# Kernel tuning notes

Hardware: AMD Instinct MI355X
Metric: run time of the kernel (lower is better)

## Reference

```python
import jax, jax.numpy as jnp
import numpy as np

BUFFER_C = 1.25

def setup_inputs() -> dict:
    key = jax.random.key(0)
    k1, k2, k3 = jax.random.split(key, 3)
    T, D, E = 4096, 1024, 8
    x = jax.random.normal(k1, (T, D), dtype=jnp.float32)
    Wg = jax.random.normal(k2, (D, E), dtype=jnp.float32) / np.sqrt(D)
    bg = jnp.zeros((E,), dtype=jnp.float32)
    W = jax.random.normal(k3, (E, D, D), dtype=jnp.float32) / np.sqrt(D)
    b = jnp.zeros((E, D), dtype=jnp.float32)
    return {"x": x, "Wg": Wg, "bg": bg, "W": W, "b": b}


def reference(x, Wg, bg, W, b):
    # Top-1 (Switch-style) routing with capacity buffer, per-expert Linear,
    # prob-weighted combine, plus load-balancing aux loss.
    T, D = x.shape
    E = W.shape[0]
    capacity = int(BUFFER_C * T / E)

    logits = x @ Wg + bg                      # [T, E]
    probs = jax.nn.softmax(logits, axis=-1)   # [T, E]
    top_idx = jnp.argmax(probs, axis=-1)      # [T]
    top_prob = jnp.take_along_axis(probs, top_idx[:, None], axis=-1)[:, 0]

    onehot = jax.nn.one_hot(top_idx, E, dtype=x.dtype)       # [T, E]
    # 1-indexed position of each token within its expert's buffer
    pos = jnp.cumsum(onehot, axis=0) * onehot                # [T, E]
    dispatch = jnp.where((onehot > 0) & (pos <= capacity), 1.0, 0.0).astype(x.dtype)

    # dense dispatch/combine equivalent of the masked per-expert loop
    xe = jnp.einsum('te,td->etd', dispatch, x)               # [E, T, D]
    ye = jnp.einsum('etd,edf->etf', xe, W) + b[:, None, :]   # [E, T, D]
    y = jnp.einsum('te,etf->tf', dispatch, ye)               # [T, D] (0 for dropped)
    out = y * top_prob[:, None]

    # aux load-balance loss: E * sum_e f_e * P_e
    f = onehot.mean(axis=0)
    P = probs.mean(axis=0)
    aux_loss = E * jnp.sum(f * P)
    return out, aux_loss
```

## Files before the change

### kernel.cpp

```cpp
#include <hip/hip_runtime.h>
#include <hip/hip_bf16.h>
#include <cstdint>

#define T_TOK 4096
#define D_DIM 1024
#define E_EXP 8
#define CAP   640
#define MAXDROP 3456
#define MT    10
#define GBLK  1024
#define NSUB  32

typedef __attribute__((ext_vector_type(8))) short short8;
typedef __attribute__((ext_vector_type(4))) float f32x4;

__device__ inline unsigned short f2bf(float f) {
    uint32_t u = __float_as_uint(f);
    u += 0x7fffu + ((u >> 16) & 1u);
    return (unsigned short)(u >> 16);
}

__device__ inline void dma16(const void* g, void* l) {
    __builtin_amdgcn_global_load_lds(
        (const __attribute__((address_space(1))) unsigned int*)g,
        (__attribute__((address_space(3))) unsigned int*)l, 16, 0, 0);
}

#define WB_TILE(e, nt, kt) ((((size_t)(e) * 16 + (nt)) * 16 + (kt)) * 4096)
#define XG_TILE(e, mt, kt) ((((size_t)(e) * MT + (mt)) * 16 + (kt)) * 4096)

__global__ __launch_bounds__(256) void prep_kernel(
    const float* __restrict__ x, const float* __restrict__ Wg,
    const float* __restrict__ bg, const float* __restrict__ W,
    unsigned short* __restrict__ Wb,
    int* __restrict__ top_idx, float* __restrict__ top_prob,
    float* __restrict__ blkpart)
{
    int bid = blockIdx.x;
    int tid = threadIdx.x;

    if (bid >= GBLK) {
        int bid2 = (bid - GBLK) * 2;
        int e   = bid2 >> 8;
        int kt  = (bid2 >> 4) & 15;
        int ntA = bid2 & 15;
        int k0  = kt * 64;
        const float* Wsrc = W + (size_t)e * D_DIM * D_DIM + (size_t)k0 * D_DIM;

        int c0 = tid, c1 = tid + 256;
        int g0 = c0 >> 6, n0c = c0 & 63;
        int g1 = c1 >> 6, n1c = c1 & 63;

        #pragma unroll
        for (int half = 0; half < 2; half++) {
            int n0 = (ntA + half) * 64;
            unsigned short* dst = Wb + WB_TILE(e, ntA + half, kt);
            const float* s0 = Wsrc + (size_t)(g0 * 8) * D_DIM + n0 + n0c;
            const float* s1 = Wsrc + (size_t)(g1 * 8) * D_DIM + n0 + n1c;
            float v[8], u[8];
            #pragma unroll
            for (int z = 0; z < 8; z++) v[z] = s0[(size_t)z * D_DIM];
            #pragma unroll
            for (int z = 0; z < 8; z++) u[z] = s1[(size_t)z * D_DIM];
            short8 a, b2;
            #pragma unroll
            for (int z = 0; z < 8; z++) { a[z] = (short)f2bf(v[z]); b2[z] = (short)f2bf(u[z]); }
            *(short8*)&dst[(size_t)c0 * 8] = a;
            *(short8*)&dst[(size_t)c1 * 8] = b2;
        }
    } else {
        __shared__ float probs_sm[4][8];
        int wid  = tid >> 6;
        int lane = tid & 63;
        int t = bid * 4 + wid;

        const float* xr = x + (size_t)t * D_DIM;

        float acc[8];
        #pragma unroll
        for (int e = 0; e < 8; e++) acc[e] = 0.f;

        #pragma unroll
        for (int ii = 0; ii < 16; ii++) {
            int d = lane + 64 * ii;
            float xv = xr[d];
            const float4* wr = (const float4*)(Wg + (size_t)d * 8);
            float4 a = wr[0], bq = wr[1];
            acc[0] += xv * a.x;  acc[1] += xv * a.y;
            acc[2] += xv * a.z;  acc[3] += xv * a.w;
            acc[4] += xv * bq.x; acc[5] += xv * bq.y;
            acc[6] += xv * bq.z; acc[7] += xv * bq.w;
        }
        #pragma unroll
        for (int off = 32; off > 0; off >>= 1) {
            #pragma unroll
            for (int e = 0; e < 8; e++) acc[e] += __shfl_xor(acc[e], off, 64);
        }
        if (lane == 0) {
            float lg[8];
            #pragma unroll
            for (int e = 0; e < 8; e++) lg[e] = acc[e] + bg[e];
            float m = lg[0]; int am = 0;
            #pragma unroll
            for (int e = 1; e < 8; e++) { if (lg[e] > m) { m = lg[e]; am = e; } }
            float ex[8], s = 0.f;
            #pragma unroll
            for (int e = 0; e < 8; e++) { ex[e] = __expf(lg[e] - m); s += ex[e]; }
            float inv = 1.f / s;
            top_idx[t]  = am;
            top_prob[t] = ex[am] * inv;
            #pragma unroll
            for (int e = 0; e < 8; e++) probs_sm[wid][e] = ex[e] * inv;
        }
        __syncthreads();
        if (tid < 8) {
            float s = probs_sm[0][tid] + probs_sm[1][tid]
                    + probs_sm[2][tid] + probs_sm[3][tid];
            blkpart[(size_t)bid * 8 + tid] = s;
        }
    }
}

__global__ __launch_bounds__(1024) void scan_kernel(
    const int* __restrict__ top_idx,
    int* __restrict__ tok_list, int* __restrict__ cnt,
    const float* __restrict__ blkpart,
    float* __restrict__ out, float* __restrict__ out_aux)
{
    __shared__ int counts[64][8];
    __shared__ int excl[64][8];
    __shared__ int fulltot[8];
    __shared__ int droplist[MAXDROP];
    __shared__ int ndrop;
    __shared__ float wpart[16][8];

    int tid  = threadIdx.x;
    int wv   = tid >> 6;
    int lane = tid & 63;
    unsigned long long ltmask = (lane == 0) ? 0ull : ((~0ull) >> (64 - lane));

    if (tid == 0) ndrop = 0;

    float p[8];
    {
        const float4* bp = (const float4*)(blkpart + (size_t)tid * 8);
        float4 p0 = bp[0], p1 = bp[1];
        p[0] = p0.x; p[1] = p0.y; p[2] = p0.z; p[3] = p0.w;
        p[4] = p1.x; p[5] = p1.y; p[6] = p1.z; p[7] = p1.w;
    }

    int ecache[4];
    #pragma unroll
    for (int c = 0; c < 4; c++)
        ecache[c] = top_idx[(4 * wv + c) * 64 + lane];

    #pragma unroll
    for (int c = 0; c < 4; c++) {
        int chunk = 4 * wv + c;
        int e = ecache[c];
        #pragma unroll
        for (int q = 0; q < 8; q++) {
            unsigned long long mk = __ballot(e == q);
            int tot = __popcll(mk);
            if (lane == q) counts[chunk][q] = tot;
        }
    }
    __syncthreads();

    if (wv == 0) {
        #pragma unroll
        for (int q = 0; q < 8; q++) {
            int v = counts[lane][q];
            int orig = v;
            #pragma unroll
            for (int off = 1; off < 64; off <<= 1) {
                int n = __shfl_up(v, off, 64);
                if (lane >= off) v += n;
            }
            excl[lane][q] = v - orig;
            int total = __shfl(v, 63, 64);
            if (lane == 0) {
                fulltot[q] = total;
                cnt[q] = total < CAP ? total : CAP;
            }
        }
    }
    __syncthreads();

    #pragma unroll
    for (int c = 0; c < 4; c++) {
        int chunk = 4 * wv + c;
        int t = chunk * 64 + lane;
        int e = ecache[c];
        int pos = 0;
        #pragma unroll
        for (int q = 0; q < 8; q++) {
            unsigned long long mk = __ballot(e == q);
            if (e == q) pos = excl[chunk][q] + __popcll(mk & ltmask);
        }
        if (pos < CAP) {
            tok_list[e * CAP + pos] = t;
        } else {
            int di = atomicAdd(&ndrop, 1);
            droplist[di] = t;
        }
    }

    #pragma unroll
    for (int off = 32; off > 0; off >>= 1) {
        #pragma unroll
        for (int e = 0; e < 8; e++) p[e] += __shfl_xor(p[e], off, 64);
    }
    if (lane == 0) {
        #pragma unroll
        for (int e = 0; e < 8; e++) wpart[wv][e] = p[e];
    }
    __syncthreads();

    int nd = ndrop;
    int grp = tid >> 8;
    int col = (tid & 255) * 4;
    float4 z = {0.f, 0.f, 0.f, 0.f};
    for (int d = grp; d < nd; d += 4) {
        int row = droplist[d];
        *(float4*)&out[(size_t)row * D_DIM + col] = z;
    }

    if (tid == 0) {
        float s = 0.f;
        #pragma unroll
        for (int e = 0; e < 8; e++) {
            float Pe = 0.f;
            #pragma unroll
            for (int w = 0; w < 16; w++) Pe += wpart[w][e];
            s += ((float)fulltot[e] / (float)T_TOK) * (Pe / (float)T_TOK);
        }
        out_aux[0] = (float)E_EXP * s;
    }
}

__global__ __launch_bounds__(256) void gather_kernel(
    const float* __restrict__ x, const int* __restrict__ tok_list,
    const int* __restrict__ cnt, unsigned short* __restrict__ xg)
{
    int bid = blockIdx.x;
    int e   = bid / (MT * 16);
    int rem = bid % (MT * 16);
    int mt  = rem >> 4, kt = rem & 15;
    int count = cnt[e];
    int m0 = mt * 64;
    if (m0 >= count) return;

    int tid = threadIdx.x;
    const int* tl = tok_list + e * CAP;
    unsigned short* dst = xg + XG_TILE(e, mt, kt);

    #pragma unroll
    for (int p = 0; p < 2; p++) {
        int c = tid + 256 * p;
        int g = c >> 6, row = c & 63;
        int gm = m0 + row;
        int tok = tl[gm < count ? gm : count - 1];
        const float* src = x + (size_t)tok * D_DIM + kt * 64 + g * 8;
        float4 v0 = *(const float4*)(src);
        float4 v1 = *(const float4*)(src + 4);
        short8 v;
        v[0] = f2bf(v0.x); v[1] = f2bf(v0.y); v[2] = f2bf(v0.z); v[3] = f2bf(v0.w);
        v[4] = f2bf(v1.x); v[5] = f2bf(v1.y); v[6] = f2bf(v1.z); v[7] = f2bf(v1.w);
        *(short8*)&dst[(size_t)c * 8] = v;
    }
}

__global__ __launch_bounds__(512) void expert_gemm(
    const unsigned short* __restrict__ xg, const unsigned short* __restrict__ Wb,
    const float* __restrict__ bias,
    const int* __restrict__ tok_list, const int* __restrict__ cnt,
    const float* __restrict__ top_prob, float* __restrict__ out)
{
    int bid = blockIdx.x;
    int e   = bid / 40;
    int rem = bid % 40;
    int mtb = rem >> 3, ntb = rem & 7;
    int count = cnt[e];
    int m0 = mtb * 128;
    if (m0 >= count) return;
    int n0 = ntb * 128;

    __shared__ unsigned short Ab[3][2][4][64][8];
    __shared__ unsigned short Bb[3][2][4][64][8];

    int tid  = threadIdx.x;
    int lane = tid & 63, w = tid >> 6;
    int quad = lane >> 4, l16 = lane & 15;
    int wr = w >> 2, wc = w & 3;

    const int* tl = tok_list + e * CAP;

    int  wa    = w & 3;
    int  shalf = wa >> 1;
    int  sg0   = (wa & 1) * 2;
    const unsigned short* sbase =
        (w < 4) ? (xg + XG_TILE(e, 2 * mtb + shalf, 0) + (size_t)lane * 8)
                : (Wb + WB_TILE(e, 2 * ntb + shalf, 0) + (size_t)lane * 8);

    #define STAGE(s, buf) do {                                                  \
        size_t off_ = (size_t)((s) >> 1) * 4096 + (size_t)((s) & 1) * 2048;     \
        if (w < 4) {                                                            \
            dma16(sbase + off_ + (size_t)sg0 * 512,       &Ab[buf][shalf][sg0][0][0]);     \
            dma16(sbase + off_ + (size_t)(sg0 + 1) * 512, &Ab[buf][shalf][sg0 + 1][0][0]); \
        } else {                                                                \
            dma16(sbase + off_ + (size_t)sg0 * 512,       &Bb[buf][shalf][sg0][0][0]);     \
            dma16(sbase + off_ + (size_t)(sg0 + 1) * 512, &Bb[buf][shalf][sg0 + 1][0][0]); \
        }                                                                       \
    } while (0)

    f32x4 acc[4][2];
    #pragma unroll
    for (int i = 0; i < 4; i++)
        #pragma unroll
        for (int j = 0; j < 2; j++)
            acc[i][j] = (f32x4){0.f, 0.f, 0.f, 0.f};

    STAGE(0, 0);
    STAGE(1, 1);

    #pragma unroll 1
    for (int s = 0; s < NSUB; s++) {
        if (s + 1 < NSUB) { asm volatile("s_waitcnt vmcnt(2)" ::: "memory"); }
        else              { asm volatile("s_waitcnt vmcnt(0)" ::: "memory"); }
        __builtin_amdgcn_s_barrier();
        __builtin_amdgcn_sched_barrier(0);

        int cur = s % 3;
        if (s + 2 < NSUB)
            STAGE(s + 2, (s + 2) % 3);

        short8 af[4], bf[2];
        #pragma unroll
        for (int i = 0; i < 4; i++)
            af[i] = *(const short8*)&Ab[cur][wr][quad][16 * i + l16][0];
        #pragma unroll
        for (int j = 0; j < 2; j++) {
            int cb = wc * 32 + 16 * j;
            bf[j] = *(const short8*)&Bb[cur][cb >> 6][quad][(cb & 63) + l16][0];
        }
        #pragma unroll
        for (int i = 0; i < 4; i++)
            #pragma unroll
            for (int j = 0; j < 2; j++)
                acc[i][j] = __builtin_amdgcn_mfma_f32_16x16x32_bf16(
                    af[i], bf[j], acc[i][j], 0, 0, 0);
    }
    #undef STAGE

    float bv[2];
    #pragma unroll
    for (int j = 0; j < 2; j++)
        bv[j] = bias[e * D_DIM + n0 + wc * 32 + 16 * j + l16];

    #pragma unroll
    for (int i = 0; i < 4; i++) {
        int rb = m0 + wr * 64 + 16 * i + quad * 4;
        #pragma unroll
        for (int r = 0; r < 4; r++) {
            int gm = rb + r;
            if (gm >= count) continue;
            int tok = tl[gm];
            float p = top_prob[tok];
            float* orow = out + (size_t)tok * D_DIM + n0 + wc * 32 + l16;
            #pragma unroll
            for (int j = 0; j < 2; j++)
                orow[16 * j] = (acc[i][j][r] + bv[j]) * p;
        }
    }
}

extern "C" void kernel_launch(void* const* d_in, const int* in_sizes, int n_in,
                              void* d_out, int out_size, void* d_ws, size_t ws_size,
                              hipStream_t stream) {
    const float* x  = (const float*)d_in[0];
    const float* Wg = (const float*)d_in[1];
    const float* bg = (const float*)d_in[2];
    const float* W  = (const float*)d_in[3];
    const float* b  = (const float*)d_in[4];
    float* out = (float*)d_out;

    char* ws = (char*)d_ws;
    unsigned short* Wb = (unsigned short*)(ws + 0);
    unsigned short* xg = (unsigned short*)(ws + 16777216);
    int*   top_idx  = (int*)(ws + 27262976);
    float* top_prob = (float*)(ws + 27279360);
    int*   tok_list = (int*)(ws + 27295744);
    int*   cnt      = (int*)(ws + 27316224);
    float* blkpart  = (float*)(ws + 27316256);

    hipLaunchKernelGGL(prep_kernel, dim3(GBLK + 1024), dim3(256), 0, stream,
                       x, Wg, bg, W, Wb, top_idx, top_prob, blkpart);
    hipLaunchKernelGGL(scan_kernel, dim3(1), dim3(1024), 0, stream,
                       top_idx, tok_list, cnt, blkpart, out, out + (size_t)T_TOK * D_DIM);
    hipLaunchKernelGGL(gather_kernel, dim3(E_EXP * MT * 16), dim3(256), 0, stream,
                       x, tok_list, cnt, xg);
    hipLaunchKernelGGL(expert_gemm, dim3(E_EXP * 5 * 8), dim3(512), 0, stream,
                       xg, Wb, b, tok_list, cnt, top_prob, out);
}
```

Baseline: 139.9 us.

## Fuse single-block routing scan into gather kernel with redundant per-block scans

Removes the single-block scan kernel and its launch. Each gather block now recomputes its expert's token positions by scanning all 4096 routing indices with one wavefront. Extra blocks handle zeroing of dropped tokens per expert and computing the counts and the aux loss. This trades a serial one-block kernel plus a launch boundary for redundant scan work spread across many blocks.

```diff
diff --git a/kernel.cpp b/kernel.cpp
--- a/kernel.cpp
+++ b/kernel.cpp
@@ -121,153 +121,143 @@
     }
 }
 
-__global__ __launch_bounds__(1024) void scan_kernel(
-    const int* __restrict__ top_idx,
+__global__ __launch_bounds__(256) void gather_kernel(
+    const float* __restrict__ x, const int* __restrict__ top_idx,
+    const float* __restrict__ blkpart,
     int* __restrict__ tok_list, int* __restrict__ cnt,
-    const float* __restrict__ blkpart,
+    unsigned short* __restrict__ xg,
     float* __restrict__ out, float* __restrict__ out_aux)
 {
-    __shared__ int counts[64][8];
-    __shared__ int excl[64][8];
-    __shared__ int fulltot[8];
-    __shared__ int droplist[MAXDROP];
-    __shared__ int ndrop;
-    __shared__ float wpart[16][8];
-
+    int bid  = blockIdx.x;
     int tid  = threadIdx.x;
-    int wv   = tid >> 6;
-    int lane = tid & 63;
+    int lane = tid & 63, wv = tid >> 6;
     unsigned long long ltmask = (lane == 0) ? 0ull : ((~0ull) >> (64 - lane));
 
-    if (tid == 0) ndrop = 0;
-
-    float p[8];
-    {
-        const float4* bp = (const float4*)(blkpart + (size_t)tid * 8);
-        float4 p0 = bp[0], p1 = bp[1];
-        p[0] = p0.x; p[1] = p0.y; p[2] = p0.z; p[3] = p0.w;
-        p[4] = p1.x; p[5] = p1.y; p[6] = p1.z; p[7] = p1.w;
-    }
-
-    int ecache[4];
-    #pragma unroll
-    for (int c = 0; c < 4; c++)
-        ecache[c] = top_idx[(4 * wv + c) * 64 + lane];
-
-    #pragma unroll
-    for (int c = 0; c < 4; c++) {
-        int chunk = 4 * wv + c;
-        int e = ecache[c];
-        #pragma unroll
-        for (int q = 0; q < 8; q++) {
-            unsigned long long mk = __ballot(e == q);
-            int tot = __popcll(mk);
-            if (lane == q) counts[chunk][q] = tot;
-        }
-    }
-    __syncthreads();
-
-    if (wv == 0) {
-        #pragma unroll
-        for (int q = 0; q < 8; q++) {
-            int v = counts[lane][q];
-            int orig = v;
-            #pragma unroll
-            for (int off = 1; off < 64; off <<= 1) {
-                int n = __shfl_up(v, off, 64);
-                if (lane >= off) v += n;
+    if (bid < E_EXP * MT * 16) {
+        __shared__ int tok_sm[64];
+        __shared__ int count_sm;
+        int e   = bid / (MT * 16);
+        int rem = bid % (MT * 16);
+        int mt  = rem >> 4, kt = rem & 15;
+        int m0  = mt * 64;
+
+        if (wv == 0) {
+            int run = 0;
+            #pragma unroll 1
+            for (int c = 0; c < 64; c++) {
+                int idxv = top_idx[c * 64 + lane];
+                unsigned long long mk = __ballot(idxv == e);
+                if (idxv == e) {
+                    int pos = run + __popcll(mk & ltmask);
+                    if (pos >= m0 && pos < m0 + 64) tok_sm[pos - m0] = c * 64 + lane;
+                }
+                run += __popcll(mk);
             }
-            excl[lane][q] = v - orig;
-            int total = __shfl(v, 63, 64);
-            if (lane == 0) {
-                fulltot[q] = total;
-                cnt[q] = total < CAP ? total : CAP;
+            if (lane == 0) count_sm = run < CAP ? run : CAP;
+        }
+        __syncthreads();
+        int count = count_sm;
+        if (m0 >= count) return;
+
+        if (wv == 0 && count < m0 + 64) {
+            int last = count - 1 - m0;
+            if (lane > last) tok_sm[lane] = tok_sm[last];
+        }
+        __syncthreads();
+
+        if (kt == 0 && tid < 64 && m0 + tid < count)
+            tok_list[e * CAP + m0 + tid] = tok_sm[tid];
+
+        unsigned short* dst = xg + XG_TILE(e, mt, kt);
+        #pragma unroll
+        for (int p = 0; p < 2; p++) {
+            int c = tid + 256 * p;
+            int g = c >> 6, row = c & 63;
+            int tok = tok_sm[row];
+            const float* src = x + (size_t)tok * D_DIM + kt * 64 + g * 8;
+            float4 v0 = *(const float4*)(src);
+            float4 v1 = *(const float4*)(src + 4);
+            short8 v;
+            v[0] = f2bf(v0.x); v[1] = f2bf(v0.y); v[2] = f2bf(v0.z); v[3] = f2bf(v0.w);
+            v[4] = f2bf(v1.x); v[5] = f2bf(v1.y); v[6] = f2bf(v1.z); v[7] = f2bf(v1.w);
+            *(short8*)&dst[(size_t)c * 8] = v;
+        }
+    } else if (bid < E_EXP * MT * 16 + E_EXP) {
+        __shared__ int droplist[MAXDROP];
+        __shared__ int ndrop;
+        int e = bid - E_EXP * MT * 16;
+        if (tid == 0) ndrop = 0;
+        __syncthreads();
+        if (wv == 0) {
+            int run = 0;
+            #pragma unroll 1
+            for (int c = 0; c < 64; c++) {
+                int idxv = top_idx[c * 64 + lane];
+                unsigned long long mk = __ballot(idxv == e);
+                if (idxv == e) {
+                    int pos = run + __popcll(mk & ltmask);
+                    if (pos >= CAP) {
+                        int di = atomicAdd(&ndrop, 1);
+                        droplist[di] = c * 64 + lane;
+                    }
+                }
+                run += __popcll(mk);
             }
         }
-    }
-    __syncthreads();
-
-    #pragma unroll
-    for (int c = 0; c < 4; c++) {
-        int chunk = 4 * wv + c;
-        int t = chunk * 64 + lane;
-        int e = ecache[c];
-        int pos = 0;
-        #pragma unroll
-        for (int q = 0; q < 8; q++) {
-            unsigned long long mk = __ballot(e == q);
-            if (e == q) pos = excl[chunk][q] + __popcll(mk & ltmask);
-        }
-        if (pos < CAP) {
-            tok_list[e * CAP + pos] = t;
-        } else {
-            int di = atomicAdd(&ndrop, 1);
-            droplist[di] = t;
-        }
-    }
-
-    #pragma unroll
-    for (int off = 32; off > 0; off >>= 1) {
-        #pragma unroll
-        for (int e = 0; e < 8; e++) p[e] += __shfl_xor(p[e], off, 64);
-    }
-    if (lane == 0) {
-        #pragma unroll
-        for (int e = 0; e < 8; e++) wpart[wv][e] = p[e];
-    }
-    __syncthreads();
-
-    int nd = ndrop;
-    int grp = tid >> 8;
-    int col = (tid & 255) * 4;
-    float4 z = {0.f, 0.f, 0.f, 0.f};
-    for (int d = grp; d < nd; d += 4) {
-        int row = droplist[d];
-        *(float4*)&out[(size_t)row * D_DIM + col] = z;
-    }
-
-    if (tid == 0) {
-        float s = 0.f;
-        #pragma unroll
-        for (int e = 0; e < 8; e++) {
-            float Pe = 0.f;
-            #pragma unroll
-            for (int w = 0; w < 16; w++) Pe += wpart[w][e];
-            s += ((float)fulltot[e] / (float)T_TOK) * (Pe / (float)T_TOK);
-        }
-        out_aux[0] = (float)E_EXP * s;
-    }
-}
-
-__global__ __launch_bounds__(256) void gather_kernel(
-    const float* __restrict__ x, const int* __restrict__ tok_list,
-    const int* __restrict__ cnt, unsigned short* __restrict__ xg)
-{
-    int bid = blockIdx.x;
-    int e   = bid / (MT * 16);
-    int rem = bid % (MT * 16);
-    int mt  = rem >> 4, kt = rem & 15;
-    int count = cnt[e];
-    int m0 = mt * 64;
-    if (m0 >= count) return;
-
-    int tid = threadIdx.x;
-    const int* tl = tok_list + e * CAP;
-    unsigned short* dst = xg + XG_TILE(e, mt, kt);
-
-    #pragma unroll
-    for (int p = 0; p < 2; p++) {
-        int c = tid + 256 * p;
-        int g = c >> 6, row = c & 63;
-        int gm = m0 + row;
-        int tok = tl[gm < count ? gm : count - 1];
-        const float* src = x + (size_t)tok * D_DIM + kt * 64 + g * 8;
-        float4 v0 = *(const float4*)(src);
-        float4 v1 = *(const float4*)(src + 4);
-        short8 v;
-        v[0] = f2bf(v0.x); v[1] = f2bf(v0.y); v[2] = f2bf(v0.z); v[3] = f2bf(v0.w);
-        v[4] = f2bf(v1.x); v[5] = f2bf(v1.y); v[6] = f2bf(v1.z); v[7] = f2bf(v1.w);
-        *(short8*)&dst[(size_t)c * 8] = v;
+        __syncthreads();
+        int nd = ndrop;
+        float4 z = {0.f, 0.f, 0.f, 0.f};
+        for (int d = 0; d < nd; d++) {
+            int row = droplist[d];
+            *(float4*)&out[(size_t)row * D_DIM + tid * 4] = z;
+        }
+    } else {
+        __shared__ float wpartP[4][8];
+        __shared__ int   wpartC[4][8];
+        __shared__ float prod[8];
+
+        float p[8]; int c8[8];
+        #pragma unroll
+        for (int e = 0; e < 8; e++) { p[e] = 0.f; c8[e] = 0; }
+
+        #pragma unroll
+        for (int r = 0; r < 4; r++) {
+            const float* bp = blkpart + (size_t)(tid * 4 + r) * 8;
+            #pragma unroll
+            for (int e = 0; e < 8; e++) p[e] += bp[e];
+        }
+        #pragma unroll
+        for (int r = 0; r < 16; r++) {
+            int idxv = top_idx[tid * 16 + r];
+            #pragma unroll
+            for (int e = 0; e < 8; e++) c8[e] += (idxv == e);
+        }
+        #pragma unroll
+        for (int off = 32; off > 0; off >>= 1) {
+            #pragma unroll
+            for (int e = 0; e < 8; e++) {
+                p[e]  += __shfl_xor(p[e], off, 64);
+                c8[e] += __shfl_xor(c8[e], off, 64);
+            }
+        }
+        if (lane == 0) {
+            #pragma unroll
+            for (int e = 0; e < 8; e++) { wpartP[wv][e] = p[e]; wpartC[wv][e] = c8[e]; }
+        }
+        __syncthreads();
+        if (tid < 8) {
+            int tot  = wpartC[0][tid] + wpartC[1][tid] + wpartC[2][tid] + wpartC[3][tid];
+            float Pe = wpartP[0][tid] + wpartP[1][tid] + wpartP[2][tid] + wpartP[3][tid];
+            cnt[tid] = tot < CAP ? tot : CAP;
+            prod[tid] = ((float)tot / (float)T_TOK) * (Pe / (float)T_TOK);
+        }
+        __syncthreads();
+        if (tid == 0) {
+            float s = 0.f;
+            #pragma unroll
+            for (int e = 0; e < 8; e++) s += prod[e];
+            out_aux[0] = (float)E_EXP * s;
+        }
     }
 }
 
@@ -396,10 +386,9 @@
 
     hipLaunchKernelGGL(prep_kernel, dim3(GBLK + 1024), dim3(256), 0, stream,
                        x, Wg, bg, W, Wb, top_idx, top_prob, blkpart);
-    hipLaunchKernelGGL(scan_kernel, dim3(1), dim3(1024), 0, stream,
-                       top_idx, tok_list, cnt, blkpart, out, out + (size_t)T_TOK * D_DIM);
-    hipLaunchKernelGGL(gather_kernel, dim3(E_EXP * MT * 16), dim3(256), 0, stream,
-                       x, tok_list, cnt, xg);
+    hipLaunchKernelGGL(gather_kernel, dim3(E_EXP * MT * 16 + E_EXP + 1), dim3(256), 0, stream,
+                       x, top_idx, blkpart, tok_list, cnt, xg,
+                       out, out + (size_t)T_TOK * D_DIM);
     hipLaunchKernelGGL(expert_gemm, dim3(E_EXP * 5 * 8), dim3(512), 0, stream,
                        xg, Wb, b, tok_list, cnt, top_prob, out);
 }
```

Result: slower. 148.1 us (+5.9%).
